# Kernel optimization log

Measured on AMD Instinct MI355X. Metric: run time of the kernel, lower is better.

## Reference

```python
import jax, jax.numpy as jnp
import numpy as np

N, C, R, K = 128, 1001, 51, 10          # rois, classes, relations, topk proposals
ROUNDS = 3                                # cfg.TEST.REL_INFER_ROUND
W_BGREL = 1.0                             # cfg.REL_INFER.NONE_BGREL_WEIGHT
W_BIN = 1.0                               # cfg.TEST.REL_INFER_BINARY_WEIGHT
MIX = 10000.0                             # scatter blending weight


def setup_inputs() -> dict:
    key = jax.random.key(0)
    k1, k2, k3 = jax.random.split(key, 3)
    # roi class scores (probabilities, positive so log is finite)
    roi_scores = jax.random.uniform(k1, (N, C), dtype=jnp.float32, minval=0.01, maxval=1.0)
    # pairwise relation log-scores (exp'd inside forward since REL_INFER.TRAIN=False)
    rel_scores = jax.random.normal(k2, (N * N, R), dtype=jnp.float32)
    # dense relationship co-occurrence matrix; channel 0 (background rel) filled with 1
    relationship_mat = jax.random.uniform(k3, (C, C, R), dtype=jnp.float32)
    relationship_mat = relationship_mat.at[:, :, 0].set(1.0)
    return {"roi_scores": roi_scores, "rel_scores": rel_scores,
            "relationship_mat": relationship_mat}


def reference(roi_scores, rel_scores, relationship_mat):
    n = roi_scores.shape[0]
    # rel_scores -> probabilities (not-train path)
    rel = jnp.exp(rel_scores).reshape(n, n, -1)          # [N,N,R]
    topk_scores, topk_labels = jax.lax.top_k(roi_scores, K)  # [N,K]
    flat = topk_labels.reshape(-1)                        # [N*K]
    # gather pairwise potentials for every (label_i, label_j) pair
    bt = relationship_mat[flat[:, None], flat[None, :]]   # [NK,NK,R]
    bt = bt.reshape(n, K, n, K, -1) * rel[:, None, :, None, :]
    # combine background relation (channel 0) with non-bg relations (MODE != 3 -> sum)
    bt = bt[..., 0] + W_BGREL * bt[..., 1:].sum(-1)       # [N,K,N,K]
    bt = (bt + bt.transpose(2, 3, 0, 1)) * 0.5            # symmetrize over roi pairs
    bt = jnp.log(bt)
    # zero the self-pair (i == j) block: torch.diagonal(bt, dim1=0, dim2=2).fill_(0)
    bt = jnp.where(jnp.eye(n, dtype=bool)[:, None, :, None], 0.0, bt)
    unary = jnp.log(topk_scores)                          # [N,K]
    Q = jnp.full((n, K), 1.0 / K, dtype=roi_scores.dtype) # softmax of ones
    for _ in range(ROUNDS):
        msg = jnp.einsum('akbl,bl->ak', bt, Q)            # mean-field message
        Q = jax.nn.softmax(W_BIN * msg + unary, axis=1)
    new_roi = jnp.zeros_like(roi_scores).at[jnp.arange(n)[:, None], topk_labels].set(Q)
    return (roi_scores + MIX * new_roi) / (1.0 + MIX)
```

## Files before the change

kernel.cpp:

```cpp
#include <hip/hip_runtime.h>
#include <hip/hip_bf16.h>

#define NN 128
#define CC 1001
#define RR 51
#define KK 10
#define NK (NN*KK)
#define BT_ELEMS (NN*KK*NN*KK)
#define W_BIN_C 1.0f
#define MIX_C 10000.0f

typedef float f4_t __attribute__((ext_vector_type(4)));
typedef f4_t f4u __attribute__((aligned(4)));

__global__ __launch_bounds__(64) void topk_kernel(const float* __restrict__ roi,
                                                  int* __restrict__ labels,
                                                  float* __restrict__ unary) {
    int a = blockIdx.x, lane = threadIdx.x;
    const float* rowp = roi + a * CC;
    float v[16];
    #pragma unroll
    for (int j = 0; j < 16; ++j) {
        int c = lane + 64 * j;
        v[j] = (c < CC) ? rowp[c] : -1e30f;
    }
    for (int k = 0; k < KK; ++k) {
        float bv = v[0]; int bj = 0;
        #pragma unroll
        for (int j = 1; j < 16; ++j) if (v[j] > bv) { bv = v[j]; bj = j; }
        int bc = lane + 64 * bj;
        #pragma unroll
        for (int m = 32; m > 0; m >>= 1) {
            float v2 = __shfl_xor(bv, m, 64);
            int   c2 = __shfl_xor(bc, m, 64);
            if (v2 > bv || (v2 == bv && c2 < bc)) { bv = v2; bc = c2; }
        }
        if (lane == (bc & 63)) {
            int j = bc >> 6;
            #pragma unroll
            for (int jj = 0; jj < 16; ++jj) if (jj == j) v[jj] = -1e30f;
        }
        if (lane == 0) {
            labels[a * KK + k] = bc;
            unary[a * KK + k]  = logf(bv);
        }
    }
}

__global__ __launch_bounds__(256) void pair_kernel(const float* __restrict__ rel_scores,
                                                   const float* __restrict__ relmat,
                                                   const int* __restrict__ labels,
                                                   float* __restrict__ bt) {
    int orig = blockIdx.x;
    int xcd = orig & 7;
    int idx = orig >> 3;
    int a = (idx >> 7) * 8 + xcd;
    int b = idx & 127;
    if (a > b) return;
    int t = threadIdx.x;
    if (a == b) {
        if (t < 100) {
            int k = t / 10, l = t % 10;
            bt[((a * KK + k) * NN + a) * KK + l] = 0.0f;
        }
        return;
    }

    __shared__ int   La[KK], Lb[KK];
    __shared__ int   baseAB[100], baseBA[100], oAB[100], oBA[100];
    __shared__ float eAB[RR], eBA[RR];

    if (t < KK)            La[t]      = labels[a * KK + t];
    else if (t < 2 * KK)   Lb[t - KK] = labels[b * KK + (t - KK)];
    if (t >= 64  && t < 64 + RR)  eAB[t - 64]  = expf(rel_scores[(a * NN + b) * RR + (t - 64)]);
    if (t >= 128 && t < 128 + RR) eBA[t - 128] = expf(rel_scores[(b * NN + a) * RR + (t - 128)]);
    __syncthreads();
    if (t < 100) {
        int k = t / 10, l = t % 10;
        baseAB[t] = (La[k] * CC + Lb[l]) * RR;
        baseBA[t] = (Lb[l] * CC + La[k]) * RR;
        oAB[t]    = ((a * KK + k) * NN + b) * KK + l;
        oBA[t]    = ((b * KK + l) * NN + a) * KK + k;
    }
    __syncthreads();

    int gid = t >> 3;
    int sub = t & 7;
    bool act0 = sub < 7, act1 = sub < 6;
    int r0 = (sub < 6) ? sub * 8 : 47;
    int r1 = sub * 8 + 4;

    f4_t zero; zero.x = zero.y = zero.z = zero.w = 0.f;
    f4_t c0A = zero, c1A = zero, c0B = zero, c1B = zero;
    if (sub < 6) {
        c0A.x = eAB[r0];   c0A.y = eAB[r0+1]; c0A.z = eAB[r0+2]; c0A.w = eAB[r0+3];
        c1A.x = eAB[r1];   c1A.y = eAB[r1+1]; c1A.z = eAB[r1+2]; c1A.w = eAB[r1+3];
        c0B.x = eBA[r0];   c0B.y = eBA[r0+1]; c0B.z = eBA[r0+2]; c0B.w = eBA[r0+3];
        c1B.x = eBA[r1];   c1B.y = eBA[r1+1]; c1B.z = eBA[r1+2]; c1B.w = eBA[r1+3];
    } else if (sub == 6) {
        c0A.x = 0.f; c0A.y = eAB[48]; c0A.z = eAB[49]; c0A.w = eAB[50];
        c0B.x = 0.f; c0B.y = eBA[48]; c0B.z = eBA[49]; c0B.w = eBA[50];
    }

    f4_t A0[4], A1[4], B0[4], B1[4];
    #pragma unroll
    for (int u = 0; u < 4; ++u) {
        int kl = gid + 32 * u;
        bool h = (kl < 100);
        int kls = h ? kl : 0;
        int bA = baseAB[kls], bB = baseBA[kls];
        A0[u] = (h && act0) ? *(const f4u*)(relmat + bA + r0) : zero;
        A1[u] = (h && act1) ? *(const f4u*)(relmat + bA + r1) : zero;
        B0[u] = (h && act0) ? *(const f4u*)(relmat + bB + r0) : zero;
        B1[u] = (h && act1) ? *(const f4u*)(relmat + bB + r1) : zero;
    }
    float s[4];
    #pragma unroll
    for (int u = 0; u < 4; ++u) {
        s[u] = A0[u].x*c0A.x + A0[u].y*c0A.y + A0[u].z*c0A.z + A0[u].w*c0A.w
             + A1[u].x*c1A.x + A1[u].y*c1A.y + A1[u].z*c1A.z + A1[u].w*c1A.w
             + B0[u].x*c0B.x + B0[u].y*c0B.y + B0[u].z*c0B.z + B0[u].w*c0B.w
             + B1[u].x*c1B.x + B1[u].y*c1B.y + B1[u].z*c1B.z + B1[u].w*c1B.w;
    }
    #pragma unroll
    for (int m = 4; m > 0; m >>= 1) {
        #pragma unroll
        for (int u = 0; u < 4; ++u) s[u] += __shfl_xor(s[u], m, 64);
    }
    if (sub == 0) {
        #pragma unroll
        for (int u = 0; u < 4; ++u) {
            int kl = gid + 32 * u;
            if (kl < 100) {
                float vv = logf(0.5f * s[u]);
                bt[oAB[kl]] = vv;
                bt[oBA[kl]] = vv;
            }
        }
    }
}

__global__ __launch_bounds__(640) void round_kernel(const float* __restrict__ bt,
                                                    const float* __restrict__ unary,
                                                    const float* __restrict__ Qin,
                                                    float* __restrict__ Qout,
                                                    int uniform) {
    int a = blockIdx.x, t = threadIdx.x;
    int wave = t >> 6, lane = t & 63;
    __shared__ float sQ[NK];
    __shared__ float smsg[KK];
    if (!uniform && t < NK / 4) ((f4_t*)sQ)[t] = ((const f4_t*)Qin)[t];
    __syncthreads();
    const f4_t* row = (const f4_t*)(bt + (a * KK + wave) * NK);
    float acc = 0.f;
    if (uniform) {
        #pragma unroll
        for (int j = 0; j < 5; ++j) {
            f4_t r = row[lane + 64 * j];
            acc += r.x + r.y + r.z + r.w;
        }
        acc *= (1.0f / (float)KK);
    } else {
        const f4_t* q4 = (const f4_t*)sQ;
        #pragma unroll
        for (int j = 0; j < 5; ++j) {
            f4_t r = row[lane + 64 * j];
            f4_t q = q4[lane + 64 * j];
            acc += r.x * q.x + r.y * q.y + r.z * q.z + r.w * q.w;
        }
    }
    #pragma unroll
    for (int m = 32; m > 0; m >>= 1) acc += __shfl_xor(acc, m, 64);
    if (lane == 0) smsg[wave] = acc;
    __syncthreads();
    if (t == 0) {
        float e[KK], m = -1e30f;
        #pragma unroll
        for (int k = 0; k < KK; ++k) {
            float v = W_BIN_C * smsg[k] + unary[a * KK + k];
            e[k] = v;
            if (v > m) m = v;
        }
        float s = 0.f;
        #pragma unroll
        for (int k = 0; k < KK; ++k) { e[k] = expf(e[k] - m); s += e[k]; }
        #pragma unroll
        for (int k = 0; k < KK; ++k) Qout[a * KK + k] = e[k] / s;
    }
}

__global__ __launch_bounds__(640) void round_out_kernel(const float* __restrict__ bt,
                                                        const float* __restrict__ unary,
                                                        const float* __restrict__ Qin,
                                                        const float* __restrict__ roi,
                                                        const int* __restrict__ labels,
                                                        float* __restrict__ out) {
    int a = blockIdx.x, t = threadIdx.x;
    int wave = t >> 6, lane = t & 63;
    __shared__ float sQ[NK];
    __shared__ float smsg[KK];
    __shared__ float sq[KK];
    __shared__ int   sL[KK];
    if (t < NK / 4) ((f4_t*)sQ)[t] = ((const f4_t*)Qin)[t];
    if (t >= 320 && t < 320 + KK) sL[t - 320] = labels[a * KK + (t - 320)];
    __syncthreads();
    const f4_t* row = (const f4_t*)(bt + (a * KK + wave) * NK);
    const f4_t* q4  = (const f4_t*)sQ;
    float acc = 0.f;
    #pragma unroll
    for (int j = 0; j < 5; ++j) {
        f4_t r = row[lane + 64 * j];
        f4_t q = q4[lane + 64 * j];
        acc += r.x * q.x + r.y * q.y + r.z * q.z + r.w * q.w;
    }
    #pragma unroll
    for (int m = 32; m > 0; m >>= 1) acc += __shfl_xor(acc, m, 64);
    if (lane == 0) smsg[wave] = acc;
    __syncthreads();
    if (t == 0) {
        float e[KK], m = -1e30f;
        #pragma unroll
        for (int k = 0; k < KK; ++k) {
            float v = W_BIN_C * smsg[k] + unary[a * KK + k];
            e[k] = v;
            if (v > m) m = v;
        }
        float s = 0.f;
        #pragma unroll
        for (int k = 0; k < KK; ++k) { e[k] = expf(e[k] - m); s += e[k]; }
        #pragma unroll
        for (int k = 0; k < KK; ++k) sq[k] = e[k] / s;
    }
    __syncthreads();
    for (int c = t; c < CC; c += 640) {
        float q = 0.f;
        #pragma unroll
        for (int k = 0; k < KK; ++k) if (sL[k] == c) q = sq[k];
        out[a * CC + c] = (roi[a * CC + c] + MIX_C * q) / (1.0f + MIX_C);
    }
}

extern "C" void kernel_launch(void* const* d_in, const int* in_sizes, int n_in,
                              void* d_out, int out_size, void* d_ws, size_t ws_size,
                              hipStream_t stream) {
    const float* roi    = (const float*)d_in[0];
    const float* rel    = (const float*)d_in[1];
    const float* relmat = (const float*)d_in[2];
    float* out = (float*)d_out;

    char* ws = (char*)d_ws;
    float* bt     = (float*)ws;
    int*   labels = (int*)(ws + (size_t)BT_ELEMS * 4);
    float* unary  = (float*)(ws + (size_t)BT_ELEMS * 4 + 5120);
    float* QA     = unary + NK;
    float* QB     = QA + NK;

    topk_kernel<<<NN, 64, 0, stream>>>(roi, labels, unary);
    pair_kernel<<<NN * NN, 256, 0, stream>>>(rel, relmat, labels, bt);
    round_kernel<<<NN, 640, 0, stream>>>(bt, unary, QA, QA, 1);
    round_kernel<<<NN, 640, 0, stream>>>(bt, unary, QA, QB, 0);
    round_out_kernel<<<NN, 640, 0, stream>>>(bt, unary, QB, roi, labels, out);
}
```

Before: 79.84 us.

## Fuse three mean-field round kernels into one cooperative kernel with grid syncs

Replaces the three separate round launches with a single cooperative kernel that runs all rounds and uses grid.sync between them. The unary values are held in registers across rounds, and each block's bt rows may stay warm in cache. This removes two kernel launch gaps. In exchange it adds cooperative launch overhead and grid-wide barrier cost, and all 128 blocks must be co-resident.

```diff
diff --git a/kernel.cpp b/kernel.cpp
--- a/kernel.cpp
+++ b/kernel.cpp
@@ -1,5 +1,8 @@
 #include <hip/hip_runtime.h>
 #include <hip/hip_bf16.h>
+#include <hip/hip_cooperative_groups.h>
+
+namespace cg = cooperative_groups;
 
 #define NN 128
 #define CC 1001
@@ -140,103 +143,126 @@
     }
 }
 
-__global__ __launch_bounds__(640) void round_kernel(const float* __restrict__ bt,
-                                                    const float* __restrict__ unary,
-                                                    const float* __restrict__ Qin,
-                                                    float* __restrict__ Qout,
-                                                    int uniform) {
-    int a = blockIdx.x, t = threadIdx.x;
-    int wave = t >> 6, lane = t & 63;
-    __shared__ float sQ[NK];
-    __shared__ float smsg[KK];
-    if (!uniform && t < NK / 4) ((f4_t*)sQ)[t] = ((const f4_t*)Qin)[t];
-    __syncthreads();
-    const f4_t* row = (const f4_t*)(bt + (a * KK + wave) * NK);
-    float acc = 0.f;
-    if (uniform) {
-        #pragma unroll
-        for (int j = 0; j < 5; ++j) {
-            f4_t r = row[lane + 64 * j];
-            acc += r.x + r.y + r.z + r.w;
-        }
-        acc *= (1.0f / (float)KK);
-    } else {
-        const f4_t* q4 = (const f4_t*)sQ;
-        #pragma unroll
-        for (int j = 0; j < 5; ++j) {
-            f4_t r = row[lane + 64 * j];
-            f4_t q = q4[lane + 64 * j];
-            acc += r.x * q.x + r.y * q.y + r.z * q.z + r.w * q.w;
-        }
-    }
-    #pragma unroll
-    for (int m = 32; m > 0; m >>= 1) acc += __shfl_xor(acc, m, 64);
-    if (lane == 0) smsg[wave] = acc;
-    __syncthreads();
-    if (t == 0) {
-        float e[KK], m = -1e30f;
-        #pragma unroll
-        for (int k = 0; k < KK; ++k) {
-            float v = W_BIN_C * smsg[k] + unary[a * KK + k];
-            e[k] = v;
-            if (v > m) m = v;
-        }
-        float s = 0.f;
-        #pragma unroll
-        for (int k = 0; k < KK; ++k) { e[k] = expf(e[k] - m); s += e[k]; }
-        #pragma unroll
-        for (int k = 0; k < KK; ++k) Qout[a * KK + k] = e[k] / s;
-    }
-}
-
-__global__ __launch_bounds__(640) void round_out_kernel(const float* __restrict__ bt,
-                                                        const float* __restrict__ unary,
-                                                        const float* __restrict__ Qin,
-                                                        const float* __restrict__ roi,
-                                                        const int* __restrict__ labels,
-                                                        float* __restrict__ out) {
+__global__ __launch_bounds__(640) void rounds_kernel(const float* __restrict__ bt,
+                                                     const float* __restrict__ unary,
+                                                     float* __restrict__ QA,
+                                                     float* __restrict__ QB,
+                                                     const float* __restrict__ roi,
+                                                     const int* __restrict__ labels,
+                                                     float* __restrict__ out) {
+    cg::grid_group grid = cg::this_grid();
     int a = blockIdx.x, t = threadIdx.x;
     int wave = t >> 6, lane = t & 63;
     __shared__ float sQ[NK];
     __shared__ float smsg[KK];
     __shared__ float sq[KK];
     __shared__ int   sL[KK];
-    if (t < NK / 4) ((f4_t*)sQ)[t] = ((const f4_t*)Qin)[t];
+
+    const f4_t* row = (const f4_t*)(bt + (a * KK + wave) * NK);
+    float un[KK];
+    if (t == 0) {
+        #pragma unroll
+        for (int k = 0; k < KK; ++k) un[k] = unary[a * KK + k];
+    }
     if (t >= 320 && t < 320 + KK) sL[t - 320] = labels[a * KK + (t - 320)];
-    __syncthreads();
-    const f4_t* row = (const f4_t*)(bt + (a * KK + wave) * NK);
-    const f4_t* q4  = (const f4_t*)sQ;
-    float acc = 0.f;
-    #pragma unroll
-    for (int j = 0; j < 5; ++j) {
-        f4_t r = row[lane + 64 * j];
-        f4_t q = q4[lane + 64 * j];
-        acc += r.x * q.x + r.y * q.y + r.z * q.z + r.w * q.w;
-    }
-    #pragma unroll
-    for (int m = 32; m > 0; m >>= 1) acc += __shfl_xor(acc, m, 64);
-    if (lane == 0) smsg[wave] = acc;
-    __syncthreads();
-    if (t == 0) {
-        float e[KK], m = -1e30f;
-        #pragma unroll
-        for (int k = 0; k < KK; ++k) {
-            float v = W_BIN_C * smsg[k] + unary[a * KK + k];
-            e[k] = v;
-            if (v > m) m = v;
-        }
-        float s = 0.f;
-        #pragma unroll
-        for (int k = 0; k < KK; ++k) { e[k] = expf(e[k] - m); s += e[k]; }
-        #pragma unroll
-        for (int k = 0; k < KK; ++k) sq[k] = e[k] / s;
-    }
-    __syncthreads();
-    for (int c = t; c < CC; c += 640) {
-        float q = 0.f;
-        #pragma unroll
-        for (int k = 0; k < KK; ++k) if (sL[k] == c) q = sq[k];
-        out[a * CC + c] = (roi[a * CC + c] + MIX_C * q) / (1.0f + MIX_C);
+
+    {
+        float acc = 0.f;
+        #pragma unroll
+        for (int j = 0; j < 5; ++j) {
+            f4_t r = row[lane + 64 * j];
+            acc += r.x + r.y + r.z + r.w;
+        }
+        acc *= (1.0f / (float)KK);
+        #pragma unroll
+        for (int m = 32; m > 0; m >>= 1) acc += __shfl_xor(acc, m, 64);
+        if (lane == 0) smsg[wave] = acc;
+        __syncthreads();
+        if (t == 0) {
+            float e[KK], mx = -1e30f;
+            #pragma unroll
+            for (int k = 0; k < KK; ++k) {
+                float v = W_BIN_C * smsg[k] + un[k];
+                e[k] = v;
+                if (v > mx) mx = v;
+            }
+            float ssum = 0.f;
+            #pragma unroll
+            for (int k = 0; k < KK; ++k) { e[k] = expf(e[k] - mx); ssum += e[k]; }
+            #pragma unroll
+            for (int k = 0; k < KK; ++k) QA[a * KK + k] = e[k] / ssum;
+        }
+    }
+    grid.sync();
+
+    {
+        if (t < NK / 4) ((f4_t*)sQ)[t] = ((const f4_t*)QA)[t];
+        __syncthreads();
+        const f4_t* q4 = (const f4_t*)sQ;
+        float acc = 0.f;
+        #pragma unroll
+        for (int j = 0; j < 5; ++j) {
+            f4_t r = row[lane + 64 * j];
+            f4_t q = q4[lane + 64 * j];
+            acc += r.x * q.x + r.y * q.y + r.z * q.z + r.w * q.w;
+        }
+        #pragma unroll
+        for (int m = 32; m > 0; m >>= 1) acc += __shfl_xor(acc, m, 64);
+        if (lane == 0) smsg[wave] = acc;
+        __syncthreads();
+        if (t == 0) {
+            float e[KK], mx = -1e30f;
+            #pragma unroll
+            for (int k = 0; k < KK; ++k) {
+                float v = W_BIN_C * smsg[k] + un[k];
+                e[k] = v;
+                if (v > mx) mx = v;
+            }
+            float ssum = 0.f;
+            #pragma unroll
+            for (int k = 0; k < KK; ++k) { e[k] = expf(e[k] - mx); ssum += e[k]; }
+            #pragma unroll
+            for (int k = 0; k < KK; ++k) QB[a * KK + k] = e[k] / ssum;
+        }
+    }
+    grid.sync();
+
+    {
+        if (t < NK / 4) ((f4_t*)sQ)[t] = ((const f4_t*)QB)[t];
+        __syncthreads();
+        const f4_t* q4 = (const f4_t*)sQ;
+        float acc = 0.f;
+        #pragma unroll
+        for (int j = 0; j < 5; ++j) {
+            f4_t r = row[lane + 64 * j];
+            f4_t q = q4[lane + 64 * j];
+            acc += r.x * q.x + r.y * q.y + r.z * q.z + r.w * q.w;
+        }
+        #pragma unroll
+        for (int m = 32; m > 0; m >>= 1) acc += __shfl_xor(acc, m, 64);
+        if (lane == 0) smsg[wave] = acc;
+        __syncthreads();
+        if (t == 0) {
+            float e[KK], mx = -1e30f;
+            #pragma unroll
+            for (int k = 0; k < KK; ++k) {
+                float v = W_BIN_C * smsg[k] + un[k];
+                e[k] = v;
+                if (v > mx) mx = v;
+            }
+            float ssum = 0.f;
+            #pragma unroll
+            for (int k = 0; k < KK; ++k) { e[k] = expf(e[k] - mx); ssum += e[k]; }
+            #pragma unroll
+            for (int k = 0; k < KK; ++k) sq[k] = e[k] / ssum;
+        }
+        __syncthreads();
+        for (int c = t; c < CC; c += 640) {
+            float q = 0.f;
+            #pragma unroll
+            for (int k = 0; k < KK; ++k) if (sL[k] == c) q = sq[k];
+            out[a * CC + c] = (roi[a * CC + c] + MIX_C * q) / (1.0f + MIX_C);
+        }
     }
 }
 
@@ -257,7 +283,9 @@
 
     topk_kernel<<<NN, 64, 0, stream>>>(roi, labels, unary);
     pair_kernel<<<NN * NN, 256, 0, stream>>>(rel, relmat, labels, bt);
-    round_kernel<<<NN, 640, 0, stream>>>(bt, unary, QA, QA, 1);
-    round_kernel<<<NN, 640, 0, stream>>>(bt, unary, QA, QB, 0);
-    round_out_kernel<<<NN, 640, 0, stream>>>(bt, unary, QB, roi, labels, out);
-}
+
+    void* args[] = {(void*)&bt, (void*)&unary, (void*)&QA, (void*)&QB,
+                    (void*)&roi, (void*)&labels, (void*)&out};
+    hipLaunchCooperativeKernel((void*)rounds_kernel, dim3(NN), dim3(640),
+                               args, 0, stream);
+}
```

Measured after the change: 118.1 us. +47.9%, slower.
